# Kernel tuning notes

Hardware: AMD Instinct MI355X
Metric: run time of the kernel (lower is better)

The kernel has to match this reference:

```python
import jax, jax.numpy as jnp
import numpy as np

N, C, T = 64, 128, 2048
S = 9          # shift_size
D = 1          # dilation
EPS = 1e-5


def setup_inputs() -> dict:
    key = jax.random.key(0)
    k1, k2 = jax.random.split(key)
    x = jax.random.normal(k1, (N, C, T), dtype=jnp.float32)
    conv_w = jax.random.normal(k2, (C, S), dtype=jnp.float32) * (1.0 / np.sqrt(S))
    gamma = jnp.ones((C,), dtype=jnp.float32)
    beta = jnp.zeros((C,), dtype=jnp.float32)
    return {"x": x, "conv_w": conv_w, "gamma": gamma, "beta": beta}


def reference(x, conv_w, gamma, beta):
    n, c, t = x.shape
    s = conv_w.shape[1]
    # --- per-channel temporal shift with zero fill (vectorized shift()) ---
    sh = ((jnp.arange(c) % s) - s // 2) * D                    # [C]
    idx = jnp.arange(t)[None, :] - sh[:, None]                 # [C, T] source index
    valid = (idx >= 0) & (idx < t)
    idxc = jnp.clip(idx, 0, t - 1)
    xs = jnp.take_along_axis(x, jnp.broadcast_to(idxc[None], (n, c, t)), axis=2)
    xs = jnp.where(valid[None], xs, 0.0)                       # [N, C, T]
    # --- zero-pad channel dim then unfold windows of size S, stride 1 (q=1) ---
    pad_top = s // 2
    pad_bot = s // 2 - (1 if s % 2 == 0 else 0)
    xp = jnp.pad(xs, ((0, 0), (pad_top, pad_bot), (0, 0)))     # [N, C+pads, T]
    win_idx = jnp.arange(c)[:, None] + jnp.arange(s)[None, :]  # [C, S]
    w = xp[:, win_idx, :]                                      # [N, C, S, T]
    # --- grouped 1x1 conv: each output channel i mixes its S-window ---
    out = jnp.einsum('ncst,cs->nct', w, conv_w)                # [N, C, T]
    # --- BatchNorm1d (training-mode batch stats, biased var) + ReLU ---
    mean = out.mean(axis=(0, 2), keepdims=True)
    var = ((out - mean) ** 2).mean(axis=(0, 2), keepdims=True)
    out = (out - mean) * jax.lax.rsqrt(var + EPS)
    out = out * gamma[None, :, None] + beta[None, :, None]
    return jax.nn.relu(out)
```

## Files before the change

kernel.cpp:

```cpp
#include <hip/hip_runtime.h>

#define NN 64
#define CC 128
#define TT 2048
#define SS 9
#define PAD 4
#define EPSF 1e-5f
#define TL 32
#define ROWS (CC + 2 * PAD)
#define STRIDE (TL + 1)
#define NB 16

__global__ __launch_bounds__(256, 8) void conv_store_stats(
    const float* __restrict__ x, const float* __restrict__ cw,
    float* __restrict__ buckets, float* __restrict__ out)
{
    __shared__ float ls[ROWS * STRIDE];
    __shared__ float sred[512];

    const int n     = blockIdx.y;
    const int t0    = blockIdx.x * TL;
    const int tid   = threadIdx.x;
    const int lane  = tid & 63;
    const int wid   = tid >> 6;
    const int col   = lane & 31;
    const int rhalf = lane >> 5;
    const float* __restrict__ xn = x + (size_t)n * CC * TT;

#pragma unroll
    for (int i = 0; i < 17; ++i) {
        const int r  = wid * 34 + 2 * i + rhalf;
        const int c2 = r - PAD;
        float v = 0.f;
        if (c2 >= 0 && c2 < CC) {
            const int sh = (c2 % SS) - PAD;
            const int t  = t0 + col - sh;
            if (t >= 0 && t < TT) v = xn[c2 * TT + t];
        }
        ls[r * STRIDE + col] = v;
    }

    const int c  = tid & (CC - 1);
    const int jb = (tid >> 7) * (TL / 2);
    float wv[SS];
#pragma unroll
    for (int s = 0; s < SS; ++s) wv[s] = cw[c * SS + s];

    __syncthreads();

    const int base = c * STRIDE + jb;
    float res[TL / 2];
    float s1 = 0.f, s2 = 0.f;
#pragma unroll
    for (int j = 0; j < TL / 2; ++j) {
        float acc = 0.f;
#pragma unroll
        for (int s = 0; s < SS; ++s)
            acc = fmaf(wv[s], ls[base + s * STRIDE + j], acc);
        res[j] = acc;
        s1 += acc;
        s2 = fmaf(acc, acc, s2);
    }

    __syncthreads();
#pragma unroll
    for (int j = 0; j < TL / 2; ++j)
        ls[c * STRIDE + jb + j] = res[j];
    sred[tid]       = s1;
    sred[256 + tid] = s2;
    __syncthreads();

    if (tid < CC) {
        float* bs = buckets + ((blockIdx.x + blockIdx.y) & (NB - 1)) * 2 * CC;
        atomicAdd(&bs[tid],      sred[tid]       + sred[tid + 128]);
        atomicAdd(&bs[CC + tid], sred[256 + tid] + sred[256 + tid + 128]);
    }

    float* __restrict__ on = out + (size_t)n * CC * TT + t0;
#pragma unroll
    for (int i = 0; i < 16; ++i) {
        const int r = wid * 32 + 2 * i + rhalf;
        on[(size_t)r * TT + col] = ls[r * STRIDE + col];
    }
}

__global__ __launch_bounds__(256, 8) void norm_relu(
    const float* __restrict__ buckets, const float* __restrict__ gamma,
    const float* __restrict__ beta, float* __restrict__ out)
{
    const int row = blockIdx.x;
    const int c   = row & (CC - 1);

    float t1 = 0.f, t2 = 0.f;
#pragma unroll
    for (int k = 0; k < NB; ++k) {
        t1 += buckets[k * 2 * CC + c];
        t2 += buckets[k * 2 * CC + CC + c];
    }
    const float inv_cnt = 1.0f / (float)(NN * TT);
    const float mean = t1 * inv_cnt;
    const float var  = t2 * inv_cnt - mean * mean;
    const float inv  = rsqrtf(var + EPSF);
    const float g = gamma[c] * inv;
    const float b = beta[c] - mean * g;

    float4* __restrict__ o4 = (float4*)(out + (size_t)row * TT);
#pragma unroll
    for (int k = 0; k < 2; ++k) {
        const int i = threadIdx.x + k * 256;
        float4 v = o4[i];
        v.x = fmaf(v.x, g, b); v.y = fmaf(v.y, g, b);
        v.z = fmaf(v.z, g, b); v.w = fmaf(v.w, g, b);
        v.x = v.x > 0.f ? v.x : 0.f;
        v.y = v.y > 0.f ? v.y : 0.f;
        v.z = v.z > 0.f ? v.z : 0.f;
        v.w = v.w > 0.f ? v.w : 0.f;
        o4[i] = v;
    }
}

extern "C" void kernel_launch(void* const* d_in, const int* in_sizes, int n_in,
                              void* d_out, int out_size, void* d_ws, size_t ws_size,
                              hipStream_t stream)
{
    const float* x     = (const float*)d_in[0];
    const float* cw    = (const float*)d_in[1];
    const float* gamma = (const float*)d_in[2];
    const float* beta  = (const float*)d_in[3];
    float* out     = (float*)d_out;
    float* buckets = (float*)d_ws;

    hipMemsetAsync(buckets, 0, (size_t)NB * 2 * CC * sizeof(float), stream);
    dim3 grid1(TT / TL, NN);
    conv_store_stats<<<grid1, 256, 0, stream>>>(x, cw, buckets, out);
    norm_relu<<<NN * CC, 256, 0, stream>>>(buckets, gamma, beta, out);
}
```

Before: 155.0 us.

## Fuse conv, batch stats, and norm+ReLU into one cooperative kernel

Adds a cooperative-groups kernel where each block computes two time tiles of the shifted grouped conv and keeps the results in registers. Per-channel sums go into atomic buckets, and a grid-wide sync follows. Each block then computes the BN scale and shift and writes normalized ReLU output directly. This removes the intermediate write and re-read of the full output tensor and the second launch, at the cost of a grid barrier, more registers per thread, and a residency requirement that is checked at launch with fallback to the old path.

```diff
diff --git a/kernel.cpp b/kernel.cpp
--- a/kernel.cpp
+++ b/kernel.cpp
@@ -1,4 +1,7 @@
 #include <hip/hip_runtime.h>
+#include <hip/hip_cooperative_groups.h>
+
+namespace cg = cooperative_groups;
 
 #define NN 64
 #define CC 128
@@ -11,6 +14,107 @@
 #define STRIDE (TL + 1)
 #define NB 16
 
+__global__ __launch_bounds__(256, 8) void fused_all(
+    const float* __restrict__ x, const float* __restrict__ cw,
+    float* __restrict__ buckets, const float* __restrict__ gamma,
+    const float* __restrict__ beta, float* __restrict__ out)
+{
+    __shared__ float ls[ROWS * STRIDE];
+
+    const int n     = blockIdx.y;
+    const int t0    = blockIdx.x * (2 * TL);
+    const int tid   = threadIdx.x;
+    const int lane  = tid & 63;
+    const int wid   = tid >> 6;
+    const int col   = lane & 31;
+    const int rhalf = lane >> 5;
+    const float* __restrict__ xn = x + (size_t)n * CC * TT;
+
+    const int c  = tid & (CC - 1);
+    const int jb = (tid >> 7) * (TL / 2);
+    float wv[SS];
+#pragma unroll
+    for (int s = 0; s < SS; ++s) wv[s] = cw[c * SS + s];
+
+    float res[2 * (TL / 2)];
+    float s1 = 0.f, s2 = 0.f;
+
+#pragma unroll
+    for (int half = 0; half < 2; ++half) {
+        const int tb = t0 + half * TL;
+
+#pragma unroll
+        for (int i = 0; i < 17; ++i) {
+            const int r  = wid * 34 + 2 * i + rhalf;
+            const int c2 = r - PAD;
+            float v = 0.f;
+            if (c2 >= 0 && c2 < CC) {
+                const int sh = (c2 % SS) - PAD;
+                const int t  = tb + col - sh;
+                if (t >= 0 && t < TT) v = xn[c2 * TT + t];
+            }
+            ls[r * STRIDE + col] = v;
+        }
+        __syncthreads();
+
+        const int base = c * STRIDE + jb;
+#pragma unroll
+        for (int j = 0; j < TL / 2; ++j) {
+            float acc = 0.f;
+#pragma unroll
+            for (int s = 0; s < SS; ++s)
+                acc = fmaf(wv[s], ls[base + s * STRIDE + j], acc);
+            res[half * (TL / 2) + j] = acc;
+            s1 += acc;
+            s2 = fmaf(acc, acc, s2);
+        }
+        __syncthreads();
+    }
+
+    float* bs = buckets + ((blockIdx.x + blockIdx.y) & (NB - 1)) * 2 * CC;
+    atomicAdd(&bs[c],      s1);
+    atomicAdd(&bs[CC + c], s2);
+
+    cg::this_grid().sync();
+
+    if (tid < CC) {
+        float t1 = 0.f, t2 = 0.f;
+#pragma unroll
+        for (int k = 0; k < NB; ++k) {
+            t1 += buckets[k * 2 * CC + tid];
+            t2 += buckets[k * 2 * CC + CC + tid];
+        }
+        const float inv_cnt = 1.0f / (float)(NN * TT);
+        const float mean = t1 * inv_cnt;
+        const float var  = t2 * inv_cnt - mean * mean;
+        const float inv  = rsqrtf(var + EPSF);
+        const float gg   = gamma[tid] * inv;
+        ls[tid]      = gg;
+        ls[CC + tid] = beta[tid] - mean * gg;
+    }
+    __syncthreads();
+    const float g = ls[c];
+    const float b = ls[CC + c];
+    __syncthreads();
+
+#pragma unroll
+    for (int half = 0; half < 2; ++half) {
+#pragma unroll
+        for (int j = 0; j < TL / 2; ++j) {
+            float v = fmaf(res[half * (TL / 2) + j], g, b);
+            ls[c * STRIDE + jb + j] = v > 0.f ? v : 0.f;
+        }
+        __syncthreads();
+        float* __restrict__ on = out + (size_t)n * CC * TT + t0 + half * TL;
+#pragma unroll
+        for (int i = 0; i < 16; ++i) {
+            const int r = wid * 32 + 2 * i + rhalf;
+            on[(size_t)r * TT + col] = ls[r * STRIDE + col];
+        }
+        __syncthreads();
+    }
+}
+
 __global__ __launch_bounds__(256, 8) void conv_store_stats(
     const float* __restrict__ x, const float* __restrict__ cw,
     float* __restrict__ buckets, float* __restrict__ out)
@@ -130,8 +234,30 @@
     float* out     = (float*)d_out;
     float* buckets = (float*)d_ws;
 
+    static int coop_ok = -1;
+    if (coop_ok < 0) {
+        int nb = 0;
+        hipError_t e = hipOccupancyMaxActiveBlocksPerMultiprocessor(
+            &nb, fused_all, 256, 0);
+        int dev = 0;
+        hipGetDevice(&dev);
+        hipDeviceProp_t prop;
+        hipGetDeviceProperties(&prop, dev);
+        const int need = (TT / (2 * TL)) * NN;
+        coop_ok = (e == hipSuccess &&
+                   (long)nb * prop.multiProcessorCount >= need) ? 1 : 0;
+    }
+
     hipMemsetAsync(buckets, 0, (size_t)NB * 2 * CC * sizeof(float), stream);
-    dim3 grid1(TT / TL, NN);
-    conv_store_stats<<<grid1, 256, 0, stream>>>(x, cw, buckets, out);
-    norm_relu<<<NN * CC, 256, 0, stream>>>(buckets, gamma, beta, out);
-}
+
+    if (coop_ok) {
+        dim3 grid(TT / (2 * TL), NN);
+        void* kargs[] = { (void*)&x, (void*)&cw, (void*)&buckets,
+                          (void*)&gamma, (void*)&beta, (void*)&out };
+        hipLaunchCooperativeKernel(fused_all, grid, dim3(256), kargs, 0, stream);
+    } else {
+        dim3 grid1(TT / TL, NN);
+        conv_store_stats<<<grid1, 256, 0, stream>>>(x, cw, buckets, out);
+        norm_relu<<<NN * CC, 256, 0, stream>>>(buckets, gamma, beta, out);
+    }
+}
```

Result: no change. 155.5 us (+0.3%).

## Vectorize intermediate stores, fold BN stats once, batch rows in norm pass

Applied to the files above, without the earlier changes.

The conv kernel now writes its tile with float4 stores instead of scalar stores. The per-channel bucket reduction and scale/shift computation move into a tiny single-block kernel, so the normalize pass no longer re-reads 16 buckets per row. The norm+ReLU kernel handles four rows per block with eight float4 loads in flight per thread, giving more memory parallelism. The cost is one extra kernel launch on the critical path.

```diff
diff --git a/kernel.cpp b/kernel.cpp
--- a/kernel.cpp
+++ b/kernel.cpp
@@ -78,44 +78,83 @@
 
     float* __restrict__ on = out + (size_t)n * CC * TT + t0;
 #pragma unroll
-    for (int i = 0; i < 16; ++i) {
-        const int r = wid * 32 + 2 * i + rhalf;
-        on[(size_t)r * TT + col] = ls[r * STRIDE + col];
+    for (int k = 0; k < 4; ++k) {
+        const int f   = tid + 256 * k;
+        const int row = f >> 3;
+        const int q   = (f & 7) * 4;
+        float4 v;
+        v.x = ls[row * STRIDE + q];
+        v.y = ls[row * STRIDE + q + 1];
+        v.z = ls[row * STRIDE + q + 2];
+        v.w = ls[row * STRIDE + q + 3];
+        *reinterpret_cast<float4*>(on + (size_t)row * TT + q) = v;
     }
 }
 
-__global__ __launch_bounds__(256, 8) void norm_relu(
+__global__ void stats_fold(
     const float* __restrict__ buckets, const float* __restrict__ gamma,
-    const float* __restrict__ beta, float* __restrict__ out)
+    const float* __restrict__ beta, float* __restrict__ gb)
 {
-    const int row = blockIdx.x;
-    const int c   = row & (CC - 1);
+    const int c = threadIdx.x;
+    if (c < CC) {
+        float t1 = 0.f, t2 = 0.f;
+#pragma unroll
+        for (int k = 0; k < NB; ++k) {
+            t1 += buckets[k * 2 * CC + c];
+            t2 += buckets[k * 2 * CC + CC + c];
+        }
+        const float inv_cnt = 1.0f / (float)(NN * TT);
+        const float mean = t1 * inv_cnt;
+        const float var  = t2 * inv_cnt - mean * mean;
+        const float inv  = rsqrtf(var + EPSF);
+        const float g = gamma[c] * inv;
+        gb[c]      = g;
+        gb[CC + c] = beta[c] - mean * g;
+    }
+}
 
-    float t1 = 0.f, t2 = 0.f;
+__global__ __launch_bounds__(256, 8) void norm_relu_vec(
+    const float* __restrict__ gb, float* __restrict__ out)
+{
+    const int r0  = blockIdx.x * 4;
+    const int tid = threadIdx.x;
+    float4* __restrict__ o4 = (float4*)out;
+
+    float g[4], b[4];
 #pragma unroll
-    for (int k = 0; k < NB; ++k) {
-        t1 += buckets[k * 2 * CC + c];
-        t2 += buckets[k * 2 * CC + CC + c];
+    for (int k = 0; k < 4; ++k) {
+        const int c = (r0 + k) & (CC - 1);
+        g[k] = gb[c];
+        b[k] = gb[CC + c];
     }
-    const float inv_cnt = 1.0f / (float)(NN * TT);
-    const float mean = t1 * inv_cnt;
-    const float var  = t2 * inv_cnt - mean * mean;
-    const float inv  = rsqrtf(var + EPSF);
-    const float g = gamma[c] * inv;
-    const float b = beta[c] - mean * g;
 
-    float4* __restrict__ o4 = (float4*)(out + (size_t)row * TT);
+    float4 v[8];
 #pragma unroll
-    for (int k = 0; k < 2; ++k) {
-        const int i = threadIdx.x + k * 256;
-        float4 v = o4[i];
-        v.x = fmaf(v.x, g, b); v.y = fmaf(v.y, g, b);
-        v.z = fmaf(v.z, g, b); v.w = fmaf(v.w, g, b);
-        v.x = v.x > 0.f ? v.x : 0.f;
-        v.y = v.y > 0.f ? v.y : 0.f;
-        v.z = v.z > 0.f ? v.z : 0.f;
-        v.w = v.w > 0.f ? v.w : 0.f;
-        o4[i] = v;
+    for (int k = 0; k < 4; ++k) {
+        const size_t base = (size_t)(r0 + k) * (TT / 4);
+        v[2 * k]     = o4[base + tid];
+        v[2 * k + 1] = o4[base + tid + 256];
+    }
+#pragma unroll
+    for (int k = 0; k < 4; ++k) {
+#pragma unroll
+        for (int j = 0; j < 2; ++j) {
+            float4& w = v[2 * k + j];
+            w.x = fmaf(w.x, g[k], b[k]);
+            w.y = fmaf(w.y, g[k], b[k]);
+            w.z = fmaf(w.z, g[k], b[k]);
+            w.w = fmaf(w.w, g[k], b[k]);
+            w.x = w.x > 0.f ? w.x : 0.f;
+            w.y = w.y > 0.f ? w.y : 0.f;
+            w.z = w.z > 0.f ? w.z : 0.f;
+            w.w = w.w > 0.f ? w.w : 0.f;
+        }
+    }
+#pragma unroll
+    for (int k = 0; k < 4; ++k) {
+        const size_t base = (size_t)(r0 + k) * (TT / 4);
+        o4[base + tid]       = v[2 * k];
+        o4[base + tid + 256] = v[2 * k + 1];
     }
 }
 
@@ -129,9 +168,12 @@
     const float* beta  = (const float*)d_in[3];
     float* out     = (float*)d_out;
     float* buckets = (float*)d_ws;
+    float* gb      = (float*)d_ws + NB * 2 * CC;
 
     hipMemsetAsync(buckets, 0, (size_t)NB * 2 * CC * sizeof(float), stream);
+
     dim3 grid1(TT / TL, NN);
     conv_store_stats<<<grid1, 256, 0, stream>>>(x, cw, buckets, out);
-    norm_relu<<<NN * CC, 256, 0, stream>>>(buckets, gamma, beta, out);
+    stats_fold<<<1, 128, 0, stream>>>(buckets, gamma, beta, gb);
+    norm_relu_vec<<<(NN * CC) / 4, 256, 0, stream>>>(gb, out);
 }
```

Measured after the change: 157.5 us. About the same (+1.6%).

## Recompute conv in second pass instead of storing and rereading intermediate output

Applied to the files above, without the earlier changes.

The first kernel now only computes the convolution to gather per-channel sum and sum-of-squares statistics, without writing the intermediate tensor. A second kernel recomputes the shifted grouped conv per tile, applies the batch-norm affine and ReLU, and writes the output once using float4 stores staged through shared memory. This replaces a full write plus read-modify-write of the output with a second read of the input, cutting global memory traffic at the cost of doing the convolution twice.

```diff
diff --git a/kernel.cpp b/kernel.cpp
--- a/kernel.cpp
+++ b/kernel.cpp
@@ -11,9 +11,10 @@
 #define STRIDE (TL + 1)
 #define NB 16
 
-__global__ __launch_bounds__(256, 8) void conv_store_stats(
+
+__global__ __launch_bounds__(256, 8) void conv_stats(
     const float* __restrict__ x, const float* __restrict__ cw,
-    float* __restrict__ buckets, float* __restrict__ out)
+    float* __restrict__ buckets)
 {
     __shared__ float ls[ROWS * STRIDE];
     __shared__ float sred[512];
@@ -49,7 +50,6 @@
     __syncthreads();
 
     const int base = c * STRIDE + jb;
-    float res[TL / 2];
     float s1 = 0.f, s2 = 0.f;
 #pragma unroll
     for (int j = 0; j < TL / 2; ++j) {
@@ -57,39 +57,38 @@
 #pragma unroll
         for (int s = 0; s < SS; ++s)
             acc = fmaf(wv[s], ls[base + s * STRIDE + j], acc);
-        res[j] = acc;
         s1 += acc;
         s2 = fmaf(acc, acc, s2);
     }
 
-    __syncthreads();
-#pragma unroll
-    for (int j = 0; j < TL / 2; ++j)
-        ls[c * STRIDE + jb + j] = res[j];
     sred[tid]       = s1;
     sred[256 + tid] = s2;
     __syncthreads();
-
     if (tid < CC) {
         float* bs = buckets + ((blockIdx.x + blockIdx.y) & (NB - 1)) * 2 * CC;
         atomicAdd(&bs[tid],      sred[tid]       + sred[tid + 128]);
         atomicAdd(&bs[CC + tid], sred[256 + tid] + sred[256 + tid + 128]);
     }
-
-    float* __restrict__ on = out + (size_t)n * CC * TT + t0;
-#pragma unroll
-    for (int i = 0; i < 16; ++i) {
-        const int r = wid * 32 + 2 * i + rhalf;
-        on[(size_t)r * TT + col] = ls[r * STRIDE + col];
-    }
 }
 
-__global__ __launch_bounds__(256, 8) void norm_relu(
+__global__ __launch_bounds__(256, 8) void conv_norm_store(
+    const float* __restrict__ x, const float* __restrict__ cw,
     const float* __restrict__ buckets, const float* __restrict__ gamma,
     const float* __restrict__ beta, float* __restrict__ out)
 {
-    const int row = blockIdx.x;
-    const int c   = row & (CC - 1);
+    __shared__ float ls[ROWS * STRIDE];
+
+    const int n     = blockIdx.y;
+    const int t0    = blockIdx.x * TL;
+    const int tid   = threadIdx.x;
+    const int lane  = tid & 63;
+    const int wid   = tid >> 6;
+    const int col   = lane & 31;
+    const int rhalf = lane >> 5;
+    const float* __restrict__ xn = x + (size_t)n * CC * TT;
+
+    const int c  = tid & (CC - 1);
+    const int jb = (tid >> 7) * (TL / 2);
 
     float t1 = 0.f, t2 = 0.f;
 #pragma unroll
@@ -104,18 +103,55 @@
     const float g = gamma[c] * inv;
     const float b = beta[c] - mean * g;
 
-    float4* __restrict__ o4 = (float4*)(out + (size_t)row * TT);
+    float wv[SS];
 #pragma unroll
-    for (int k = 0; k < 2; ++k) {
-        const int i = threadIdx.x + k * 256;
-        float4 v = o4[i];
-        v.x = fmaf(v.x, g, b); v.y = fmaf(v.y, g, b);
-        v.z = fmaf(v.z, g, b); v.w = fmaf(v.w, g, b);
-        v.x = v.x > 0.f ? v.x : 0.f;
-        v.y = v.y > 0.f ? v.y : 0.f;
-        v.z = v.z > 0.f ? v.z : 0.f;
-        v.w = v.w > 0.f ? v.w : 0.f;
-        o4[i] = v;
+    for (int s = 0; s < SS; ++s) wv[s] = cw[c * SS + s];
+
+#pragma unroll
+    for (int i = 0; i < 17; ++i) {
+        const int r  = wid * 34 + 2 * i + rhalf;
+        const int c2 = r - PAD;
+        float v = 0.f;
+        if (c2 >= 0 && c2 < CC) {
+            const int sh = (c2 % SS) - PAD;
+            const int t  = t0 + col - sh;
+            if (t >= 0 && t < TT) v = xn[c2 * TT + t];
+        }
+        ls[r * STRIDE + col] = v;
+    }
+    __syncthreads();
+
+    const int base = c * STRIDE + jb;
+    float res[TL / 2];
+#pragma unroll
+    for (int j = 0; j < TL / 2; ++j) {
+        float acc = 0.f;
+#pragma unroll
+        for (int s = 0; s < SS; ++s)
+            acc = fmaf(wv[s], ls[base + s * STRIDE + j], acc);
+        res[j] = acc;
+    }
+    __syncthreads();
+
+#pragma unroll
+    for (int j = 0; j < TL / 2; ++j) {
+        float v = fmaf(res[j], g, b);
+        ls[c * STRIDE + jb + j] = v > 0.f ? v : 0.f;
+    }
+    __syncthreads();
+
+    float* __restrict__ on = out + (size_t)n * CC * TT + t0;
+#pragma unroll
+    for (int k = 0; k < 4; ++k) {
+        const int f   = tid + 256 * k;
+        const int row = f >> 3;
+        const int q   = (f & 7) * 4;
+        float4 v;
+        v.x = ls[row * STRIDE + q];
+        v.y = ls[row * STRIDE + q + 1];
+        v.z = ls[row * STRIDE + q + 2];
+        v.w = ls[row * STRIDE + q + 3];
+        *reinterpret_cast<float4*>(on + (size_t)row * TT + q) = v;
     }
 }
 
@@ -131,7 +167,8 @@
     float* buckets = (float*)d_ws;
 
     hipMemsetAsync(buckets, 0, (size_t)NB * 2 * CC * sizeof(float), stream);
-    dim3 grid1(TT / TL, NN);
-    conv_store_stats<<<grid1, 256, 0, stream>>>(x, cw, buckets, out);
-    norm_relu<<<NN * CC, 256, 0, stream>>>(buckets, gamma, beta, out);
+
+    dim3 grid(TT / TL, NN);
+    conv_stats<<<grid, 256, 0, stream>>>(x, cw, buckets);
+    conv_norm_store<<<grid, 256, 0, stream>>>(x, cw, buckets, gamma, beta, out);
 }
```

Measured after the change: 153.1 us. No clear change (-1.2%).
